# Kernel tuning notes

Hardware: AMD Instinct MI355X
Metric: run time of the kernel (lower is better)

Reference implementation:

```python
import jax, jax.numpy as jnp
import numpy as np

T, B, A, D, P = 2048, 1024, 4, 128, 256  # timesteps, batch, n_actions, d, n_participants


def setup_inputs() -> dict:
    key = jax.random.key(0)
    ks = jax.random.split(key, 8)
    # one-hot chosen action per (t, b)
    act_idx = jax.random.randint(ks[0], (T, B), 0, A)
    actions = jax.nn.one_hot(act_idx, A, dtype=jnp.float32)            # [T,B,A]
    rewards = jax.random.uniform(ks[1], (T, B, A), dtype=jnp.float32)  # [T,B,A]
    pid = jax.random.randint(ks[2], (B,), 0, P).astype(jnp.float32)    # [B]
    pid_col = jnp.broadcast_to(pid[None, :, None], (T, B, 1))
    inputs = jnp.concatenate([actions, rewards, pid_col], axis=-1)[:, None]  # [T,1,B,2A+1]
    s = 0.5
    return {
        'inputs': inputs,
        'phi_raw': s * jax.random.normal(ks[3], (P, D), dtype=jnp.float32),
        'chi_raw': s * jax.random.normal(ks[4], (P, D), dtype=jnp.float32),
        'beta_raw': s * jax.random.normal(ks[5], (P, D), dtype=jnp.float32),
        'kappa_raw': s * jax.random.normal(ks[6], (P, D), dtype=jnp.float32),
        'C_raw': s * jax.random.normal(ks[7], (P, D, D), dtype=jnp.float32),
    }


def reference(inputs, phi_raw, chi_raw, beta_raw, kappa_raw, C_raw):
    x = jnp.nan_to_num(inputs[:, 0], nan=0.0)        # [T,B,F]
    nA = (x.shape[-1] - 1) // 2
    actions = x[..., :nA]                            # [T,B,A]
    rewards = x[..., nA:2 * nA]                      # [T,B,A]
    pids = x[0, :, -1].astype(jnp.int32)             # [B]

    # per-participant constrained params, gathered once per sequence
    phi = jnp.clip(jax.nn.sigmoid(phi_raw), 0.01, 0.99)[pids][:, None, :]    # [B,1,D]
    chi = jnp.clip(jax.nn.sigmoid(chi_raw), 0.01, 0.99)[pids][:, None, :]
    beta = jnp.clip(jax.nn.softplus(beta_raw), 0.1, 10.0)[pids][:, None, :]
    kappa = jnp.clip(kappa_raw, -10.0, 10.0)[pids][:, None, :]
    C = jnp.clip(C_raw, -10.0, 10.0)[pids]                                   # [B,D,D]

    bsz = x.shape[1]
    q0 = jnp.full((bsz, nA, phi.shape[-1]), 0.5, dtype=x.dtype)  # [B,A,D]
    h0 = jnp.zeros_like(q0)

    def step(carry, at_rt):
        q, h = carry
        a_t, r_t = at_rt                      # [B,A] each
        q = (1.0 - phi) * q + phi * (r_t * a_t)[..., None]
        h = (1.0 - chi) * h + chi * a_t[..., None]
        logit = ((beta * q).sum(-1) + (kappa * h).sum(-1)
                 + jnp.einsum('bad,bde,bae->ba', h, C, q))  # [B,A]
        return (q, h), logit

    (q, h), logits = jax.lax.scan(step, (q0, h0), (actions, rewards))
    logits = logits[:, None]                  # [T,1,B,A] (batch_first=False)
    return logits, q, h
```

## Files before the change

### kernel.cpp

```cpp
#include <hip/hip_runtime.h>
#include <stdint.h>

#define T_DIM 2048
#define B_DIM 1024
#define A_DIM 4
#define D_DIM 128
#define TC 32
#define NCHUNK (T_DIM / TC)
#define LDH 136
#define LDC 136
#define HB_BYTES (128 * LDH * 2)
#define QT_S 65
#define SMEM_BYTES (HB_BYTES + 128 * QT_S * 4)

typedef __attribute__((ext_vector_type(8))) short bf16x8;
typedef __attribute__((ext_vector_type(4))) float f32x4;

__device__ __forceinline__ float clampf(float x, float lo, float hi) {
    return fminf(fmaxf(x, lo), hi);
}
__device__ __forceinline__ uint16_t bf16rnd(float f) {
    uint32_t u = __builtin_bit_cast(uint32_t, f) + 0x8000u;
    return (uint16_t)(u >> 16);
}
__device__ __forceinline__ uint32_t pack2(float x, float y) {
    uint32_t ux = __builtin_bit_cast(uint32_t, x) + 0x8000u;
    uint32_t uy = __builtin_bit_cast(uint32_t, y) + 0x8000u;
    return __builtin_amdgcn_perm(uy, ux, 0x07060302);
}
__device__ __forceinline__ float bfLO(uint32_t u) {
    return __builtin_bit_cast(float, u << 16);
}
__device__ __forceinline__ float bfHI(uint32_t u) {
    return __builtin_bit_cast(float, u & 0xFFFF0000u);
}
template <int CTRL>
__device__ __forceinline__ float dppadd(float x) {
    int xi = __builtin_bit_cast(int, x);
    int yi = __builtin_amdgcn_mov_dpp(xi, CTRL, 0xF, 0xF, false);
    return x + __builtin_bit_cast(float, yi);
}
__device__ __forceinline__ float rowsum16(float x) {
    x = dppadd<0x121>(x);
    x = dppadd<0x122>(x);
    x = dppadd<0x124>(x);
    x = dppadd<0x128>(x);
    return x;
}

__global__ __launch_bounds__(256, 2)
void gql_fused(const float* __restrict__ inp,
               const float* __restrict__ phi_raw,
               const float* __restrict__ chi_raw,
               const float* __restrict__ beta_raw,
               const float* __restrict__ kappa_raw,
               const float* __restrict__ C_raw,
               float* __restrict__ out)
{
    __shared__ __attribute__((aligned(16))) char smem[SMEM_BYTES];

    const int b    = blockIdx.x;
    const int tid  = threadIdx.x;
    const int lane = tid & 63;
    const int wv   = tid >> 6;
    const int ml   = lane & 15;
    const int qd   = lane >> 4;

    const int pid = (int)inp[(size_t)b * 9 + 8];

    const int d0 = lane * 2;
    float2 pr = *(const float2*)(phi_raw + (size_t)pid * D_DIM + d0);
    float2 cr = *(const float2*)(chi_raw + (size_t)pid * D_DIM + d0);
    float phi0 = clampf(1.f / (1.f + __expf(-pr.x)), 0.01f, 0.99f);
    float phi1 = clampf(1.f / (1.f + __expf(-pr.y)), 0.01f, 0.99f);
    float chi0 = clampf(1.f / (1.f + __expf(-cr.x)), 0.01f, 0.99f);
    float chi1 = clampf(1.f / (1.f + __expf(-cr.y)), 0.01f, 0.99f);
    float omphi0 = 1.f - phi0, omphi1 = 1.f - phi1;
    float omchi0 = 1.f - chi0, omchi1 = 1.f - chi1;

    float breg[9];
    #pragma unroll
    for (int nt = 0; nt < 8; ++nt) {
        float x = beta_raw[(size_t)pid * D_DIM + nt * 16 + ml];
        breg[nt] = clampf(log1pf(__expf(x)), 0.1f, 10.0f);
    }
    breg[8] = 0.f;

    {
        uint16_t* Ct = (uint16_t*)smem;
        const float* Cp = C_raw + (size_t)pid * (D_DIM * D_DIM);
        #pragma unroll 8
        for (int i = 0; i < 64; ++i) {
            int idx = i * 256 + tid;
            int d = idx >> 7, e = idx & 127;
            Ct[e * LDC + d] = bf16rnd(clampf(Cp[idx], -10.f, 10.f));
        }
        for (int i = tid; i < 16 * LDC; i += 256) {
            int n = i / LDC;
            int k = i - n * LDC;
            float v = (n == 0 && k < D_DIM)
                        ? clampf(kappa_raw[(size_t)pid * D_DIM + k], -10.f, 10.f) : 0.f;
            Ct[(128 + n) * LDC + k] = bf16rnd(v);
        }
    }
    __syncthreads();

    bf16x8 bfr[9][4];
    {
        const uint16_t* Ct = (const uint16_t*)smem;
        #pragma unroll
        for (int nt = 0; nt < 9; ++nt)
            #pragma unroll
            for (int kt = 0; kt < 4; ++kt)
                bfr[nt][kt] = *(const bf16x8*)&Ct[(nt * 16 + ml) * LDC + kt * 32 + qd * 8];
    }
    __syncthreads();

    uint32_t* H32 = (uint32_t*)smem;
    uint32_t* Qt  = (uint32_t*)(smem + HB_BYTES);
    const uint16_t* Hb16 = (const uint16_t*)smem;
    const int SWt = ((lane >> 4) & 3) << 3;

    float actv, rav;
    {
        size_t t = (size_t)(lane & 31);
        const float* p = inp + (t * B_DIM + b) * 9;
        float a = p[wv], r = p[4 + wv];
        actv = a; rav = a * r;
    }

    float q0 = 0.5f, q1 = 0.5f, h0 = 0.f, h1 = 0.f;

    for (int chunk = 0; chunk < NCHUNK; ++chunk) {
        const int ai = __builtin_bit_cast(int, actv);
        const int ri = __builtin_bit_cast(int, rav);

        uint32_t hw_prev = 0, qwA0 = 0, qwA1 = 0;
        float q0p = 0.f, q1p = 0.f;
        #pragma unroll
        for (int tl = 0; tl < TC; ++tl) {
            float sa = __builtin_bit_cast(float, __builtin_amdgcn_readlane(ai, tl));
            float sr = __builtin_bit_cast(float, __builtin_amdgcn_readlane(ri, tl));
            q0 = fmaf(omphi0, q0, phi0 * sr);
            q1 = fmaf(omphi1, q1, phi1 * sr);
            h0 = fmaf(omchi0, h0, chi0 * sa);
            h1 = fmaf(omchi1, h1, chi1 * sa);
            uint32_t hw = pack2(h0, h1);
            if (tl & 1) {
                int m = wv * TC + tl - 1;
                H32[m * 68 + lane] = hw_prev;
                H32[(m + 1) * 68 + lane] = hw;
            } else {
                hw_prev = hw;
            }
            if ((tl & 1) == 0) {
                q0p = q0; q1p = q1;
            } else if ((tl & 3) == 1) {
                qwA0 = pack2(q0p, q0);
                qwA1 = pack2(q1p, q1);
            } else {
                uint32_t qwB0 = pack2(q0p, q0);
                uint32_t qwB1 = pack2(q1p, q1);
                int m2  = wv * 16 + ((tl - 3) >> 1);
                int adw = d0 * QT_S + (m2 ^ SWt);
                Qt[adw]     = qwA0;  Qt[adw + 1]        = qwB0;
                Qt[adw + QT_S] = qwA1; Qt[adw + QT_S + 1] = qwB1;
            }
        }

        if (chunk + 1 < NCHUNK) {
            size_t t = (size_t)(chunk + 1) * TC + (lane & 31);
            const float* p = inp + (t * B_DIM + b) * 9;
            float a = p[wv], r = p[4 + wv];
            actv = a; rav = a * r;
        }

        #pragma unroll
        for (int mi = 0; mi < 2; ++mi) {
            const int mt = wv * 2 + mi;
            f32x4 acc[9];
            #pragma unroll
            for (int nt = 0; nt < 9; ++nt) acc[nt] = (f32x4){0.f, 0.f, 0.f, 0.f};

            #pragma unroll
            for (int kt = 0; kt < 4; ++kt) {
                bf16x8 afr = *(const bf16x8*)&Hb16[(size_t)(mt * 16 + ml) * LDH + kt * 32 + qd * 8];
                #pragma unroll
                for (int nt = 0; nt < 9; ++nt)
                    acc[nt] = __builtin_amdgcn_mfma_f32_16x16x32_bf16(afr, bfr[nt][kt], acc[nt], 0, 0, 0);
            }

            bool km = (ml == 0);
            float p0 = km ? acc[8][0] : 0.f;
            float p1 = km ? acc[8][1] : 0.f;
            float p2 = km ? acc[8][2] : 0.f;
            float p3 = km ? acc[8][3] : 0.f;

            const int m2e = mt * 8 + qd * 2;
            #pragma unroll
            for (int nt = 0; nt < 8; ++nt) {
                const int SWc = ((nt >> 1) & 3) << 3;
                int adw = (nt * 16 + ml) * QT_S + (m2e ^ SWc);
                uint32_t w0 = Qt[adw];
                uint32_t w1 = Qt[adw + 1];
                float g0 = acc[nt][0] + breg[nt];
                float g1 = acc[nt][1] + breg[nt];
                float g2 = acc[nt][2] + breg[nt];
                float g3 = acc[nt][3] + breg[nt];
                p0 = fmaf(g0, bfLO(w0), p0);
                p1 = fmaf(g1, bfHI(w0), p1);
                p2 = fmaf(g2, bfLO(w1), p2);
                p3 = fmaf(g3, bfHI(w1), p3);
            }

            p0 = rowsum16(p0);
            p1 = rowsum16(p1);
            p2 = rowsum16(p2);
            p3 = rowsum16(p3);

            if (ml == 0) {
                int row0 = mt * 16 + qd * 4;
                #pragma unroll
                for (int r = 0; r < 4; ++r) {
                    int row = row0 + r;
                    int aa = row >> 5;
                    int tl = row & (TC - 1);
                    size_t t = (size_t)chunk * TC + tl;
                    float pv = (r == 0) ? p0 : (r == 1) ? p1 : (r == 2) ? p2 : p3;
                    out[(t * B_DIM + b) * A_DIM + aa] = pv;
                }
            }
        }
    }

    size_t qbase = (size_t)T_DIM * B_DIM * A_DIM;
    size_t off = (size_t)b * (A_DIM * D_DIM) + (size_t)wv * D_DIM + d0;
    *(float2*)&out[qbase + off] = make_float2(q0, q1);
    *(float2*)&out[qbase + (size_t)B_DIM * A_DIM * D_DIM + off] = make_float2(h0, h1);
}

extern "C" void kernel_launch(void* const* d_in, const int* in_sizes, int n_in,
                              void* d_out, int out_size, void* d_ws, size_t ws_size,
                              hipStream_t stream) {
    const float* inp    = (const float*)d_in[0];
    const float* phi_r  = (const float*)d_in[1];
    const float* chi_r  = (const float*)d_in[2];
    const float* beta_r = (const float*)d_in[3];
    const float* kap_r  = (const float*)d_in[4];
    const float* C_r    = (const float*)d_in[5];
    float* outp = (float*)d_out;
    gql_fused<<<dim3(B_DIM), dim3(256), 0, stream>>>(inp, phi_r, chi_r, beta_r, kap_r, C_r, outp);
}
```

Baseline: 610.3 us.

## Rescale recurrence states and fold phi/chi into C, kappa and beta weights

The recurrences now track q/phi and h/chi, so each step does one FMA per element instead of a multiply plus an FMA. The phi and chi scales are folded into the bf16 C matrix, the kappa row and the beta vector, and beta is used as the MFMA accumulator's initial value rather than added afterwards. Float-to-bf16 packing now uses the hardware v_cvt_pk_bf16_f32 instruction. Unscaled states can reach magnitudes up to 1/phi, which may change bf16 rounding behaviour, and an extra shared-memory staging step plus a __syncthreads are added in the prologue.

New measurement: 762.5 us. +24.9%, slower.

```diff
diff --git a/kernel.cpp b/kernel.cpp
--- a/kernel.cpp
+++ b/kernel.cpp
@@ -23,10 +23,10 @@
     uint32_t u = __builtin_bit_cast(uint32_t, f) + 0x8000u;
     return (uint16_t)(u >> 16);
 }
-__device__ __forceinline__ uint32_t pack2(float x, float y) {
-    uint32_t ux = __builtin_bit_cast(uint32_t, x) + 0x8000u;
-    uint32_t uy = __builtin_bit_cast(uint32_t, y) + 0x8000u;
-    return __builtin_amdgcn_perm(uy, ux, 0x07060302);
+__device__ __forceinline__ uint32_t cvtpk(float lo, float hi) {
+    uint32_t r;
+    asm("v_cvt_pk_bf16_f32 %0, %1, %2" : "=v"(r) : "v"(lo), "v"(hi));
+    return r;
 }
 __device__ __forceinline__ float bfLO(uint32_t u) {
     return __builtin_bit_cast(float, u << 16);
@@ -78,11 +78,21 @@
     float omphi0 = 1.f - phi0, omphi1 = 1.f - phi1;
     float omchi0 = 1.f - chi0, omchi1 = 1.f - chi1;
 
+    float* sphi = (float*)(smem + 61440);
+    float* schi = sphi + 128;
+    if (tid < 128) {
+        sphi[tid] = clampf(1.f / (1.f + __expf(-phi_raw[(size_t)pid * D_DIM + tid])), 0.01f, 0.99f);
+    } else {
+        int k = tid - 128;
+        schi[k] = clampf(1.f / (1.f + __expf(-chi_raw[(size_t)pid * D_DIM + k])), 0.01f, 0.99f);
+    }
+    __syncthreads();
+
     float breg[9];
     #pragma unroll
     for (int nt = 0; nt < 8; ++nt) {
         float x = beta_raw[(size_t)pid * D_DIM + nt * 16 + ml];
-        breg[nt] = clampf(log1pf(__expf(x)), 0.1f, 10.0f);
+        breg[nt] = clampf(log1pf(__expf(x)), 0.1f, 10.0f) * sphi[nt * 16 + ml];
     }
     breg[8] = 0.f;
 
@@ -93,14 +103,14 @@
         for (int i = 0; i < 64; ++i) {
             int idx = i * 256 + tid;
             int d = idx >> 7, e = idx & 127;
-            Ct[e * LDC + d] = bf16rnd(clampf(Cp[idx], -10.f, 10.f));
+            Ct[e * LDC + d] = bf16rnd(clampf(Cp[idx], -10.f, 10.f) * schi[d] * sphi[e]);
         }
         for (int i = tid; i < 16 * LDC; i += 256) {
             int n = i / LDC;
             int k = i - n * LDC;
-            float v = (n == 0 && k < D_DIM)
-                        ? clampf(kappa_raw[(size_t)pid * D_DIM + k], -10.f, 10.f) : 0.f;
-            Ct[(128 + n) * LDC + k] = bf16rnd(v);
+            float kv = (n == 0 && k < D_DIM)
+                        ? clampf(kappa_raw[(size_t)pid * D_DIM + k], -10.f, 10.f) * schi[k] : 0.f;
+            Ct[(128 + n) * LDC + k] = bf16rnd(kv);
         }
     }
     __syncthreads();
@@ -129,23 +139,23 @@
         actv = a; rav = a * r;
     }
 
-    float q0 = 0.5f, q1 = 0.5f, h0 = 0.f, h1 = 0.f;
+    float u0 = 0.5f / phi0, u1 = 0.5f / phi1, v0 = 0.f, v1 = 0.f;
 
     for (int chunk = 0; chunk < NCHUNK; ++chunk) {
         const int ai = __builtin_bit_cast(int, actv);
         const int ri = __builtin_bit_cast(int, rav);
 
         uint32_t hw_prev = 0, qwA0 = 0, qwA1 = 0;
-        float q0p = 0.f, q1p = 0.f;
+        float u0p = 0.f, u1p = 0.f;
         #pragma unroll
         for (int tl = 0; tl < TC; ++tl) {
             float sa = __builtin_bit_cast(float, __builtin_amdgcn_readlane(ai, tl));
             float sr = __builtin_bit_cast(float, __builtin_amdgcn_readlane(ri, tl));
-            q0 = fmaf(omphi0, q0, phi0 * sr);
-            q1 = fmaf(omphi1, q1, phi1 * sr);
-            h0 = fmaf(omchi0, h0, chi0 * sa);
-            h1 = fmaf(omchi1, h1, chi1 * sa);
-            uint32_t hw = pack2(h0, h1);
+            u0 = fmaf(omphi0, u0, sr);
+            u1 = fmaf(omphi1, u1, sr);
+            v0 = fmaf(omchi0, v0, sa);
+            v1 = fmaf(omchi1, v1, sa);
+            uint32_t hw = cvtpk(v0, v1);
             if (tl & 1) {
                 int m = wv * TC + tl - 1;
                 H32[m * 68 + lane] = hw_prev;
@@ -154,13 +164,13 @@
                 hw_prev = hw;
             }
             if ((tl & 1) == 0) {
-                q0p = q0; q1p = q1;
+                u0p = u0; u1p = u1;
             } else if ((tl & 3) == 1) {
-                qwA0 = pack2(q0p, q0);
-                qwA1 = pack2(q1p, q1);
+                qwA0 = cvtpk(u0p, u0);
+                qwA1 = cvtpk(u1p, u1);
             } else {
-                uint32_t qwB0 = pack2(q0p, q0);
-                uint32_t qwB1 = pack2(q1p, q1);
+                uint32_t qwB0 = cvtpk(u0p, u0);
+                uint32_t qwB1 = cvtpk(u1p, u1);
                 int m2  = wv * 16 + ((tl - 3) >> 1);
                 int adw = d0 * QT_S + (m2 ^ SWt);
                 Qt[adw]     = qwA0;  Qt[adw + 1]        = qwB0;
@@ -180,7 +190,8 @@
             const int mt = wv * 2 + mi;
             f32x4 acc[9];
             #pragma unroll
-            for (int nt = 0; nt < 9; ++nt) acc[nt] = (f32x4){0.f, 0.f, 0.f, 0.f};
+            for (int nt = 0; nt < 9; ++nt)
+                acc[nt] = (f32x4){breg[nt], breg[nt], breg[nt], breg[nt]};
 
             #pragma unroll
             for (int kt = 0; kt < 4; ++kt) {
@@ -203,14 +214,10 @@
                 int adw = (nt * 16 + ml) * QT_S + (m2e ^ SWc);
                 uint32_t w0 = Qt[adw];
                 uint32_t w1 = Qt[adw + 1];
-                float g0 = acc[nt][0] + breg[nt];
-                float g1 = acc[nt][1] + breg[nt];
-                float g2 = acc[nt][2] + breg[nt];
-                float g3 = acc[nt][3] + breg[nt];
-                p0 = fmaf(g0, bfLO(w0), p0);
-                p1 = fmaf(g1, bfHI(w0), p1);
-                p2 = fmaf(g2, bfLO(w1), p2);
-                p3 = fmaf(g3, bfHI(w1), p3);
+                p0 = fmaf(acc[nt][0], bfLO(w0), p0);
+                p1 = fmaf(acc[nt][1], bfHI(w0), p1);
+                p2 = fmaf(acc[nt][2], bfLO(w1), p2);
+                p3 = fmaf(acc[nt][3], bfHI(w1), p3);
             }
 
             p0 = rowsum16(p0);
@@ -235,8 +242,8 @@
 
     size_t qbase = (size_t)T_DIM * B_DIM * A_DIM;
     size_t off = (size_t)b * (A_DIM * D_DIM) + (size_t)wv * D_DIM + d0;
-    *(float2*)&out[qbase + off] = make_float2(q0, q1);
-    *(float2*)&out[qbase + (size_t)B_DIM * A_DIM * D_DIM + off] = make_float2(h0, h1);
+    *(float2*)&out[qbase + off] = make_float2(phi0 * u0, phi1 * u1);
+    *(float2*)&out[qbase + (size_t)B_DIM * A_DIM * D_DIM + off] = make_float2(chi0 * v0, chi1 * v1);
 }
 
 extern "C" void kernel_launch(void* const* d_in, const int* in_sizes, int n_in,
```

## Split each time chunk into two half-chunks to halve LDS and raise occupancy

Applied to the files above, without the earlier changes.

Each 32-step chunk is now processed as two 16-step halves: the recurrence writes H and Q staging for 16 steps, then each wave runs a single MFMA tile over its own rows before the next half. This cuts the LDS staging buffers roughly in half and raises the launch-bounds target from 2 to 4 blocks per SM, aiming for more concurrent blocks to hide the serial recurrence latency. The trade-off is twice as many recurrence/MFMA phase switches per chunk and tighter register pressure, which could cause spills. The SMEM size now comes from the C-staging region (144*LDC), which is not shown and may need checking.

After: 2.361 ms. 3.87x slower.

```diff
diff --git a/kernel.cpp b/kernel.cpp
--- a/kernel.cpp
+++ b/kernel.cpp
@@ -6,12 +6,13 @@
 #define A_DIM 4
 #define D_DIM 128
 #define TC 32
+#define HTC 16
 #define NCHUNK (T_DIM / TC)
 #define LDH 136
 #define LDC 136
-#define HB_BYTES (128 * LDH * 2)
-#define QT_S 65
-#define SMEM_BYTES (HB_BYTES + 128 * QT_S * 4)
+#define HB_BYTES (64 * LDH * 2)
+#define QT_S 33
+#define SMEM_BYTES (144 * LDC * 2)
 
 typedef __attribute__((ext_vector_type(8))) short bf16x8;
 typedef __attribute__((ext_vector_type(4))) float f32x4;
@@ -48,7 +49,7 @@
     return x;
 }
 
-__global__ __launch_bounds__(256, 2)
+__global__ __launch_bounds__(256, 4)
 void gql_fused(const float* __restrict__ inp,
                const float* __restrict__ phi_raw,
                const float* __restrict__ chi_raw,
@@ -135,56 +136,56 @@
         const int ai = __builtin_bit_cast(int, actv);
         const int ri = __builtin_bit_cast(int, rav);
 
-        uint32_t hw_prev = 0, qwA0 = 0, qwA1 = 0;
-        float q0p = 0.f, q1p = 0.f;
         #pragma unroll
-        for (int tl = 0; tl < TC; ++tl) {
-            float sa = __builtin_bit_cast(float, __builtin_amdgcn_readlane(ai, tl));
-            float sr = __builtin_bit_cast(float, __builtin_amdgcn_readlane(ri, tl));
-            q0 = fmaf(omphi0, q0, phi0 * sr);
-            q1 = fmaf(omphi1, q1, phi1 * sr);
-            h0 = fmaf(omchi0, h0, chi0 * sa);
-            h1 = fmaf(omchi1, h1, chi1 * sa);
-            uint32_t hw = pack2(h0, h1);
-            if (tl & 1) {
-                int m = wv * TC + tl - 1;
-                H32[m * 68 + lane] = hw_prev;
-                H32[(m + 1) * 68 + lane] = hw;
-            } else {
-                hw_prev = hw;
-            }
-            if ((tl & 1) == 0) {
-                q0p = q0; q1p = q1;
-            } else if ((tl & 3) == 1) {
-                qwA0 = pack2(q0p, q0);
-                qwA1 = pack2(q1p, q1);
-            } else {
-                uint32_t qwB0 = pack2(q0p, q0);
-                uint32_t qwB1 = pack2(q1p, q1);
-                int m2  = wv * 16 + ((tl - 3) >> 1);
-                int adw = d0 * QT_S + (m2 ^ SWt);
-                Qt[adw]     = qwA0;  Qt[adw + 1]        = qwB0;
-                Qt[adw + QT_S] = qwA1; Qt[adw + QT_S + 1] = qwB1;
-            }
-        }
-
-        if (chunk + 1 < NCHUNK) {
-            size_t t = (size_t)(chunk + 1) * TC + (lane & 31);
-            const float* p = inp + (t * B_DIM + b) * 9;
-            float a = p[wv], r = p[4 + wv];
-            actv = a; rav = a * r;
-        }
-
-        #pragma unroll
-        for (int mi = 0; mi < 2; ++mi) {
-            const int mt = wv * 2 + mi;
+        for (int hf = 0; hf < 2; ++hf) {
+            uint32_t hw_prev = 0, qwA0 = 0, qwA1 = 0;
+            float q0p = 0.f, q1p = 0.f;
+            #pragma unroll
+            for (int tlh = 0; tlh < HTC; ++tlh) {
+                const int tl = hf * HTC + tlh;
+                float sa = __builtin_bit_cast(float, __builtin_amdgcn_readlane(ai, tl));
+                float sr = __builtin_bit_cast(float, __builtin_amdgcn_readlane(ri, tl));
+                q0 = fmaf(omphi0, q0, phi0 * sr);
+                q1 = fmaf(omphi1, q1, phi1 * sr);
+                h0 = fmaf(omchi0, h0, chi0 * sa);
+                h1 = fmaf(omchi1, h1, chi1 * sa);
+                uint32_t hw = pack2(h0, h1);
+                if (tlh & 1) {
+                    int m = wv * HTC + tlh - 1;
+                    H32[m * 68 + lane] = hw_prev;
+                    H32[(m + 1) * 68 + lane] = hw;
+                } else {
+                    hw_prev = hw;
+                }
+                if ((tlh & 1) == 0) {
+                    q0p = q0; q1p = q1;
+                } else if ((tlh & 3) == 1) {
+                    qwA0 = pack2(q0p, q0);
+                    qwA1 = pack2(q1p, q1);
+                } else {
+                    uint32_t qwB0 = pack2(q0p, q0);
+                    uint32_t qwB1 = pack2(q1p, q1);
+                    int m2  = wv * 8 + ((tlh - 3) >> 1);
+                    int adw = d0 * QT_S + (m2 ^ SWt);
+                    Qt[adw]     = qwA0;  Qt[adw + 1]        = qwB0;
+                    Qt[adw + QT_S] = qwA1; Qt[adw + QT_S + 1] = qwB1;
+                }
+            }
+
+            if (hf == 0 && chunk + 1 < NCHUNK) {
+                size_t t = (size_t)(chunk + 1) * TC + (lane & 31);
+                const float* p = inp + (t * B_DIM + b) * 9;
+                float a = p[wv], r = p[4 + wv];
+                actv = a; rav = a * r;
+            }
+
             f32x4 acc[9];
             #pragma unroll
             for (int nt = 0; nt < 9; ++nt) acc[nt] = (f32x4){0.f, 0.f, 0.f, 0.f};
 
             #pragma unroll
             for (int kt = 0; kt < 4; ++kt) {
-                bf16x8 afr = *(const bf16x8*)&Hb16[(size_t)(mt * 16 + ml) * LDH + kt * 32 + qd * 8];
+                bf16x8 afr = *(const bf16x8*)&Hb16[(size_t)(wv * HTC + ml) * LDH + kt * 32 + qd * 8];
                 #pragma unroll
                 for (int nt = 0; nt < 9; ++nt)
                     acc[nt] = __builtin_amdgcn_mfma_f32_16x16x32_bf16(afr, bfr[nt][kt], acc[nt], 0, 0, 0);
@@ -196,7 +197,7 @@
             float p2 = km ? acc[8][2] : 0.f;
             float p3 = km ? acc[8][3] : 0.f;
 
-            const int m2e = mt * 8 + qd * 2;
+            const int m2e = wv * 8 + qd * 2;
             #pragma unroll
             for (int nt = 0; nt < 8; ++nt) {
                 const int SWc = ((nt >> 1) & 3) << 3;
@@ -219,15 +220,12 @@
             p3 = rowsum16(p3);
 
             if (ml == 0) {
-                int row0 = mt * 16 + qd * 4;
+                int r0 = qd * 4;
                 #pragma unroll
                 for (int r = 0; r < 4; ++r) {
-                    int row = row0 + r;
-                    int aa = row >> 5;
-                    int tl = row & (TC - 1);
-                    size_t t = (size_t)chunk * TC + tl;
+                    size_t t = (size_t)chunk * TC + hf * HTC + r0 + r;
                     float pv = (r == 0) ? p0 : (r == 1) ? p1 : (r == 2) ? p2 : p3;
-                    out[(t * B_DIM + b) * A_DIM + aa] = pv;
+                    out[(t * B_DIM + b) * A_DIM + wv] = pv;
                 }
             }
         }
```
